# Kernel tuning notes

Hardware: AMD Instinct MI355X
Metric: run time of the kernel (lower is better)

The kernel has to match this reference:

```python
import jax, jax.numpy as jnp
import numpy as np

N_USERS = 60000
N_ITEMS = 30000
N_NODES = N_USERS + N_ITEMS
D = 64
L = 2


def _norm_adj(edge_index):
    # symmetrize: A_idx = [e, e.flip(0)]
    src = jnp.concatenate([edge_index[0], edge_index[1]])
    dst = jnp.concatenate([edge_index[1], edge_index[0]])
    ones = jnp.ones_like(src, dtype=jnp.float32)
    deg = jax.ops.segment_sum(ones, src, num_segments=N_NODES)
    deg = jnp.clip(deg, 1.0, None)
    val = jax.lax.rsqrt(deg[src]) * jax.lax.rsqrt(deg[dst])
    return src, dst, val


def _spmm(src, dst, val, x):
    # out[i] = sum_{(i,j) in E} val_ij * x[j]
    return jax.ops.segment_sum(val[:, None] * x[dst], src, num_segments=N_NODES)


def setup_inputs() -> dict:
    key = jax.random.key(0)
    ks = jax.random.split(key, 20)
    s = 0.02
    inp = {
        'x_txt': jax.random.normal(ks[0], (N_ITEMS, 768), jnp.float32),
        'x_img': jax.random.normal(ks[1], (N_ITEMS, 512), jnp.float32),
        'x_struct': jax.random.normal(ks[2], (N_ITEMS, 128), jnp.float32),
        'user_emb': jax.random.normal(ks[3], (3, N_USERS, D), jnp.float32) * s,
        'W_txt': jax.random.normal(ks[4], (3, 768, D), jnp.float32) * s,
        'b_txt': jax.random.normal(ks[5], (3, D), jnp.float32) * s,
        'W_img': jax.random.normal(ks[6], (3, 512, D), jnp.float32) * s,
        'b_img': jax.random.normal(ks[7], (3, D), jnp.float32) * s,
        'W_st': jax.random.normal(ks[8], (3, 128, D), jnp.float32) * s,
        'b_st': jax.random.normal(ks[9], (3, D), jnp.float32) * s,
        'Wu1': jax.random.normal(ks[10], (3 * D, 128), jnp.float32) * s,
        'bu1': jax.random.normal(ks[11], (128,), jnp.float32) * s,
        'Wu2': jax.random.normal(ks[12], (128, 3), jnp.float32) * s,
        'bu2': jax.random.normal(ks[13], (3,), jnp.float32) * s,
        'Wi1': jax.random.normal(ks[14], (3 * D, 128), jnp.float32) * s,
        'bi1': jax.random.normal(ks[15], (128,), jnp.float32) * s,
        'Wi2': jax.random.normal(ks[16], (128, 3), jnp.float32) * s,
        'bi2': jax.random.normal(ks[17], (3,), jnp.float32) * s,
        'edge_index': jax.random.randint(ks[18], (2, 500000), 0, N_NODES, jnp.int64),
    }
    return inp


def reference(x_txt, x_img, x_struct, user_emb, W_txt, b_txt, W_img, b_img,
              W_st, b_st, Wu1, bu1, Wu2, bu2, Wi1, bi1, Wi2, bi2, edge_index):
    src, dst, val = _norm_adj(edge_index)

    # item embeddings for all 3 branches at once: [n_items, 3, d]
    i0 = (jnp.einsum('nt,btd->nbd', x_txt, W_txt) + b_txt
          + jnp.einsum('nt,btd->nbd', x_img, W_img) + b_img
          + jnp.einsum('nt,btd->nbd', x_struct, W_st) + b_st)
    u0 = jnp.transpose(user_emb, (1, 0, 2))  # [n_users, 3, d]
    x = jnp.concatenate([u0, i0], axis=0).reshape(N_NODES, 3 * D)

    out = x
    for _ in range(L):
        x = _spmm(src, dst, val, x)
        out = out + x
    out = out / (L + 1)

    stack = out.reshape(N_NODES, 3, D)
    U_stack, I_stack = stack[:N_USERS], stack[N_USERS:]
    U_cat = U_stack.reshape(N_USERS, 3 * D)
    I_cat = I_stack.reshape(N_ITEMS, 3 * D)

    a_u = jax.nn.softmax(jax.nn.relu(U_cat @ Wu1 + bu1) @ Wu2 + bu2, axis=-1)
    a_i = jax.nn.softmax(jax.nn.relu(I_cat @ Wi1 + bi1) @ Wi2 + bi2, axis=-1)

    U = jnp.einsum('nb,nbd->nd', a_u, U_stack)
    I = jnp.einsum('nb,nbd->nd', a_i, I_stack)
    return jnp.concatenate([U, I], axis=0)  # [N_NODES, d]
```

## Files before the change

### kernel.cpp

```cpp
#include <hip/hip_runtime.h>
#include <math.h>

#define N_USERS 60000
#define N_ITEMS 30000
#define N_NODES 90000
#define DD 64
#define FF 192
#define FH 96
#define KK_TOT 1408
#define E_UND 500000
#define E_DIR 1000000
#define SCAN_NBLK 88

typedef __attribute__((ext_vector_type(8))) __bf16 bf16x8;
typedef __attribute__((ext_vector_type(8))) unsigned short u16x8;
typedef __attribute__((ext_vector_type(4))) float f32x4;

__device__ __forceinline__ unsigned short f2bf(float f) {
    unsigned int u = __float_as_uint(f);
    unsigned int r = (u + 0x7FFFu + ((u >> 16) & 1u)) >> 16;
    return (unsigned short)r;
}
__device__ __forceinline__ float bf_lo(unsigned int x) { return __uint_as_float(x << 16); }
__device__ __forceinline__ float bf_hi(unsigned int x) { return __uint_as_float(x & 0xFFFF0000u); }
__device__ __forceinline__ float bf2f(unsigned short x) {
    return __uint_as_float((unsigned int)x << 16);
}
__device__ __forceinline__ unsigned int pack2(float a, float b) {
    return ((unsigned int)f2bf(b) << 16) | (unsigned int)f2bf(a);
}

__global__ void k_mode(const int* __restrict__ ei, int* __restrict__ mode) {
    __shared__ int any;
    if (threadIdx.x == 0) any = 0;
    __syncthreads();
    if (ei[2 * threadIdx.x + 1] != 0) atomicOr(&any, 1);
    __syncthreads();
    if (threadIdx.x == 0) mode[0] = (any == 0) ? 1 : 0;
}

__device__ __forceinline__ void load_pair(const int* __restrict__ ei, int md, int u,
                                          int& a, int& b) {
    if (md) { a = ei[2 * u]; b = ei[2 * (E_UND + u)]; }
    else    { a = ei[u];     b = ei[E_UND + u]; }
}

__global__ void k_deg(const int* __restrict__ ei, const int* __restrict__ mode,
                      int* __restrict__ deg) {
    int i = blockIdx.x * 256 + threadIdx.x;
    if (i >= E_UND) return;
    int md = mode[0];
    int a, b;
    load_pair(ei, md, i, a, b);
    atomicAdd(&deg[a], 1);
    atomicAdd(&deg[b], 1);
}

__global__ __launch_bounds__(1024) void k_scan1(const int* __restrict__ deg,
                                                int* __restrict__ offs,
                                                int* __restrict__ bsum) {
    __shared__ int tmp[1024];
    int b = blockIdx.x, t = threadIdx.x;
    int i = b * 1024 + t;
    int v = (i < N_NODES) ? deg[i] : 0;
    tmp[t] = v;
    __syncthreads();
    for (int off = 1; off < 1024; off <<= 1) {
        int add = (t >= off) ? tmp[t - off] : 0;
        __syncthreads();
        tmp[t] += add;
        __syncthreads();
    }
    offs[i] = tmp[t] - v;
    if (t == 1023) bsum[b] = tmp[t];
}

__global__ void k_scan2(const int* __restrict__ bsum, int* __restrict__ bscan) {
    if (threadIdx.x == 0) {
        int run = 0;
        for (int b = 0; b < SCAN_NBLK; b++) { bscan[b] = run; run += bsum[b]; }
    }
}

__global__ void k_scan3(const int* __restrict__ deg, int* __restrict__ offs,
                        const int* __restrict__ bscan, int* __restrict__ cursor,
                        float* __restrict__ rsq) {
    int i = blockIdx.x * 256 + threadIdx.x;
    if (i >= N_NODES) return;
    int o = offs[i] + bscan[i >> 10];
    offs[i] = o;
    cursor[i] = o;
    int dg = deg[i];
    if (dg < 1) dg = 1;
    rsq[i] = rsqrtf((float)dg);
}

__global__ void k_fill(const int* __restrict__ ei, const int* __restrict__ mode,
                       int* __restrict__ cursor, const float* __restrict__ rsq,
                       int* __restrict__ edst, float* __restrict__ eval) {
    int i = blockIdx.x * 256 + threadIdx.x;
    if (i >= E_DIR) return;
    int md = mode[0];
    int u = (i < E_UND) ? i : i - E_UND;
    int a, b;
    load_pair(ei, md, u, a, b);
    int s, d;
    if (i < E_UND) { s = a; d = b; } else { s = b; d = a; }
    int slot = atomicAdd(&cursor[s], 1);
    edst[slot] = d;
    eval[slot] = rsq[s] * rsq[d];
}

__global__ void k_users(const float* __restrict__ ue, float* __restrict__ S,
                        unsigned short* __restrict__ Xbs) {
    int idx = blockIdx.x * 256 + threadIdx.x;
    if (idx >= N_USERS * FF) return;
    int n = idx / FF;
    int r = idx - n * FF;
    int b = r >> 6, d = r & 63;
    float v = ue[((size_t)b * N_USERS + n) * DD + d];
    S[idx] = v;
    Xbs[idx] = f2bf(v);
}

__global__ void k_cvt_w(const float* __restrict__ Wt, const float* __restrict__ Wi,
                        const float* __restrict__ Wst, unsigned short* __restrict__ Wtb) {
    int idx = blockIdx.x * 256 + threadIdx.x;
    if (idx >= FF * KK_TOT) return;
    int n = idx / KK_TOT;
    int k = idx - n * KK_TOT;
    int b = n >> 6, d = n & 63;
    float v;
    if (k < 768)       v = Wt [((size_t)b * 768 + k) * 64 + d];
    else if (k < 1280) v = Wi [((size_t)b * 512 + (k - 768)) * 64 + d];
    else               v = Wst[((size_t)b * 128 + (k - 1280)) * 64 + d];
    Wtb[idx] = f2bf(v);
}

__global__ void k_cvt_w1(const float* __restrict__ Wu1, const float* __restrict__ Wi1,
                         unsigned short* __restrict__ W1Tu,
                         unsigned short* __restrict__ W1Ti) {
    int idx = blockIdx.x * 256 + threadIdx.x;
    if (idx >= 128 * FF) return;
    int n = idx / FF;
    int k = idx - n * FF;
    W1Tu[idx] = f2bf(Wu1[(size_t)k * 128 + n]);
    W1Ti[idx] = f2bf(Wi1[(size_t)k * 128 + n]);
}

#define BM 64
#define BNH 96
#define BK 64
#define LDK 72

__global__ __launch_bounds__(256) void k_item_gemm_mfma3(
    const float* __restrict__ xt, const float* __restrict__ xi, const float* __restrict__ xs,
    const unsigned short* __restrict__ Wtb,
    const float* __restrict__ bt, const float* __restrict__ bi, const float* __restrict__ bst,
    float* __restrict__ S, unsigned short* __restrict__ Xbs) {
    __shared__ unsigned short Ash[BM * LDK];
    __shared__ unsigned short Bsh[BNH * LDK];
    const int tid  = threadIdx.x;
    const int wave = tid >> 6;
    const int lane = tid & 63;
    const int row0 = (blockIdx.x >> 1) * BM;
    const int n0   = (blockIdx.x & 1) * BNH;

    f32x4 acc[6];
#pragma unroll
    for (int tn = 0; tn < 6; tn++) acc[tn] = (f32x4){0.f, 0.f, 0.f, 0.f};

    const int l16  = lane & 15;
    const int quad = lane >> 4;

    for (int k0 = 0; k0 < KK_TOT; k0 += BK) {
#pragma unroll
        for (int i = 0; i < 2; i++) {
            int id = tid + i * 256;
            int r = id >> 3;
            int c = (id & 7) << 3;
            int gr = row0 + r;
            int gk = k0 + c;
            float4 v0 = make_float4(0.f, 0.f, 0.f, 0.f);
            float4 v1 = v0;
            if (gr < N_ITEMS) {
                const float* src;
                int kl;
                if (gk < 768)       { src = xt + (size_t)gr * 768; kl = gk; }
                else if (gk < 1280) { src = xi + (size_t)gr * 512; kl = gk - 768; }
                else                { src = xs + (size_t)gr * 128; kl = gk - 1280; }
                v0 = *(const float4*)(src + kl);
                v1 = *(const float4*)(src + kl + 4);
            }
            u16x8 pk;
            pk[0] = f2bf(v0.x); pk[1] = f2bf(v0.y); pk[2] = f2bf(v0.z); pk[3] = f2bf(v0.w);
            pk[4] = f2bf(v1.x); pk[5] = f2bf(v1.y); pk[6] = f2bf(v1.z); pk[7] = f2bf(v1.w);
            *(u16x8*)(&Ash[r * LDK + c]) = pk;
        }
#pragma unroll
        for (int i = 0; i < 3; i++) {
            int id = tid + i * 256;
            int r = id >> 3;
            int c = (id & 7) << 3;
            *(u16x8*)(&Bsh[r * LDK + c]) =
                *(const u16x8*)(&Wtb[(size_t)(n0 + r) * KK_TOT + k0 + c]);
        }
        __syncthreads();
#pragma unroll
        for (int kk = 0; kk < BK; kk += 32) {
            bf16x8 af = *(const bf16x8*)(&Ash[(wave * 16 + l16) * LDK + kk + quad * 8]);
#pragma unroll
            for (int tn = 0; tn < 6; tn++) {
                bf16x8 bfr = *(const bf16x8*)(&Bsh[(tn * 16 + l16) * LDK + kk + quad * 8]);
                acc[tn] = __builtin_amdgcn_mfma_f32_16x16x32_bf16(af, bfr, acc[tn], 0, 0, 0);
            }
        }
        __syncthreads();
    }

#pragma unroll
    for (int tn = 0; tn < 6; tn++) {
        int n = n0 + tn * 16 + l16;
        int b = n >> 6, d = n & 63;
        float bias = bt[b * 64 + d] + bi[b * 64 + d] + bst[b * 64 + d];
#pragma unroll
        for (int r = 0; r < 4; r++) {
            int row = row0 + wave * 16 + quad * 4 + r;
            if (row < N_ITEMS) {
                size_t o = (size_t)(N_USERS + row) * FF + n;
                float v = acc[tn][r] + bias;
                S[o] = v;
                Xbs[o] = f2bf(v);
            }
        }
    }
}

__global__ __launch_bounds__(192) void k_spmm_bf(const unsigned int* __restrict__ Xb,
                                                 unsigned int* __restrict__ Yb,
                                                 float* __restrict__ S,
                                                 const int* __restrict__ offs,
                                                 const int* __restrict__ deg,
                                                 const int* __restrict__ edst,
                                                 const float* __restrict__ eval) {
    int t = threadIdx.x;
    int half = (t >= FH) ? 1 : 0;
    int c = t - half * FH;
    int n = blockIdx.x * 2 + half;
    int start = offs[n];
    int dg = deg[n];
    const int* ed = edst + start;
    const float* ev = eval + start;
    float a0 = 0.f, a1 = 0.f;
    for (int j = 0; j < dg; j += 4) {
        int last = dg - 1;
        int j1 = (j + 1 < dg) ? j + 1 : last;
        int j2 = (j + 2 < dg) ? j + 2 : last;
        int j3 = (j + 3 < dg) ? j + 3 : last;
        int d0 = ed[j], d1 = ed[j1], d2 = ed[j2], d3 = ed[j3];
        float v0 = ev[j];
        float v1 = (j + 1 < dg) ? ev[j1] : 0.f;
        float v2 = (j + 2 < dg) ? ev[j2] : 0.f;
        float v3 = (j + 3 < dg) ? ev[j3] : 0.f;
        unsigned int x0 = Xb[(size_t)d0 * FH + c];
        unsigned int x1 = Xb[(size_t)d1 * FH + c];
        unsigned int x2 = Xb[(size_t)d2 * FH + c];
        unsigned int x3 = Xb[(size_t)d3 * FH + c];
        a0 = fmaf(v0, bf_lo(x0), a0); a1 = fmaf(v0, bf_hi(x0), a1);
        a0 = fmaf(v1, bf_lo(x1), a0); a1 = fmaf(v1, bf_hi(x1), a1);
        a0 = fmaf(v2, bf_lo(x2), a0); a1 = fmaf(v2, bf_hi(x2), a1);
        a0 = fmaf(v3, bf_lo(x3), a0); a1 = fmaf(v3, bf_hi(x3), a1);
    }
    size_t o = (size_t)n * FH + c;
    Yb[o] = pack2(a0, a1);
    float2* Sp = (float2*)(S + (size_t)n * FF);
    float2 s = Sp[c];
    s.x += a0; s.y += a1;
    Sp[c] = s;
}

#define LDA 200

__global__ __launch_bounds__(256) void k_attn_mfma(
    const float* __restrict__ S,
    const unsigned short* __restrict__ W1T,
    const float* __restrict__ B1,
    const float* __restrict__ W2,
    const float* __restrict__ B2,
    float* __restrict__ out,
    int node_base, int n_rows) {
    __shared__ unsigned short Atile[64 * LDA];
    __shared__ float aws[64][4];
    const int tid  = threadIdx.x;
    const int wave = tid >> 6;
    const int lane = tid & 63;
    const int row0 = blockIdx.x * 64;
    const float inv3 = 1.f / 3.f;

#pragma unroll
    for (int i = 0; i < 6; i++) {
        int id = tid + i * 256;
        int r = id / 24;
        int c = (id - r * 24) * 8;
        u16x8 pk;
        if (row0 + r < n_rows) {
            const float* src = S + (size_t)(node_base + row0 + r) * FF + c;
            float4 v0 = *(const float4*)(src);
            float4 v1 = *(const float4*)(src + 4);
            pk[0] = f2bf(v0.x * inv3); pk[1] = f2bf(v0.y * inv3);
            pk[2] = f2bf(v0.z * inv3); pk[3] = f2bf(v0.w * inv3);
            pk[4] = f2bf(v1.x * inv3); pk[5] = f2bf(v1.y * inv3);
            pk[6] = f2bf(v1.z * inv3); pk[7] = f2bf(v1.w * inv3);
        } else {
            pk = (u16x8){0, 0, 0, 0, 0, 0, 0, 0};
        }
        *(u16x8*)(&Atile[r * LDA + c]) = pk;
    }
    __syncthreads();

    f32x4 acc[8];
#pragma unroll
    for (int tn = 0; tn < 8; tn++) acc[tn] = (f32x4){0.f, 0.f, 0.f, 0.f};
    const int l16 = lane & 15;
    const int quad = lane >> 4;
#pragma unroll
    for (int kk = 0; kk < FF; kk += 32) {
        bf16x8 af = *(const bf16x8*)(&Atile[(wave * 16 + l16) * LDA + kk + quad * 8]);
#pragma unroll
        for (int tn = 0; tn < 8; tn++) {
            bf16x8 bf = *(const bf16x8*)(&W1T[(size_t)(tn * 16 + l16) * FF + kk + quad * 8]);
            acc[tn] = __builtin_amdgcn_mfma_f32_16x16x32_bf16(af, bf, acc[tn], 0, 0, 0);
        }
    }

    float pl[4][3];
#pragma unroll
    for (int r = 0; r < 4; r++) { pl[r][0] = 0.f; pl[r][1] = 0.f; pl[r][2] = 0.f; }
#pragma unroll
    for (int tn = 0; tn < 8; tn++) {
        int col = tn * 16 + l16;
        float b1v = B1[col];
        float w0 = W2[col * 3 + 0], w1 = W2[col * 3 + 1], w2v = W2[col * 3 + 2];
#pragma unroll
        for (int r = 0; r < 4; r++) {
            float h = fmaxf(acc[tn][r] + b1v, 0.f);
            pl[r][0] = fmaf(h, w0, pl[r][0]);
            pl[r][1] = fmaf(h, w1, pl[r][1]);
            pl[r][2] = fmaf(h, w2v, pl[r][2]);
        }
    }
#pragma unroll
    for (int m = 1; m <= 8; m <<= 1) {
#pragma unroll
        for (int r = 0; r < 4; r++) {
            pl[r][0] += __shfl_xor(pl[r][0], m, 64);
            pl[r][1] += __shfl_xor(pl[r][1], m, 64);
            pl[r][2] += __shfl_xor(pl[r][2], m, 64);
        }
    }
    float b20 = B2[0], b21 = B2[1], b22 = B2[2];
    if (l16 == 0) {
#pragma unroll
        for (int r = 0; r < 4; r++) {
            float l0 = pl[r][0] + b20, l1 = pl[r][1] + b21, l2 = pl[r][2] + b22;
            float mx = fmaxf(l0, fmaxf(l1, l2));
            float e0 = __expf(l0 - mx), e1 = __expf(l1 - mx), e2 = __expf(l2 - mx);
            float inv = 1.f / (e0 + e1 + e2);
            int rr = wave * 16 + quad * 4 + r;
            aws[rr][0] = e0 * inv; aws[rr][1] = e1 * inv; aws[rr][2] = e2 * inv;
        }
    }
    __syncthreads();

#pragma unroll
    for (int i = 0; i < 16; i++) {
        int flat = tid + i * 256;
        int r = flat >> 6, d = flat & 63;
        if (row0 + r < n_rows) {
            float a0 = aws[r][0], a1 = aws[r][1], a2 = aws[r][2];
            const unsigned short* Ar = &Atile[r * LDA];
            float v = a0 * bf2f(Ar[d]) + a1 * bf2f(Ar[64 + d]) + a2 * bf2f(Ar[128 + d]);
            out[(size_t)(node_base + row0 + r) * DD + d] = v;
        }
    }
}

extern "C" void kernel_launch(void* const* d_in, const int* in_sizes, int n_in,
                              void* d_out, int out_size, void* d_ws, size_t ws_size,
                              hipStream_t stream) {
    (void)in_sizes; (void)n_in; (void)out_size; (void)ws_size;
    const float* x_txt    = (const float*)d_in[0];
    const float* x_img    = (const float*)d_in[1];
    const float* x_struct = (const float*)d_in[2];
    const float* user_emb = (const float*)d_in[3];
    const float* W_txt    = (const float*)d_in[4];
    const float* b_txt    = (const float*)d_in[5];
    const float* W_img    = (const float*)d_in[6];
    const float* b_img    = (const float*)d_in[7];
    const float* W_st     = (const float*)d_in[8];
    const float* b_st     = (const float*)d_in[9];
    const float* Wu1      = (const float*)d_in[10];
    const float* bu1      = (const float*)d_in[11];
    const float* Wu2      = (const float*)d_in[12];
    const float* bu2      = (const float*)d_in[13];
    const float* Wi1      = (const float*)d_in[14];
    const float* bi1      = (const float*)d_in[15];
    const float* Wi2      = (const float*)d_in[16];
    const float* bi2      = (const float*)d_in[17];
    const int*   ei       = (const int*)d_in[18];
    float* out = (float*)d_out;

    char* base = (char*)d_ws;
    size_t off = 0;
    auto take = [&](size_t bytes) -> void* {
        void* p = base + off;
        off += (bytes + 255) & ~(size_t)255;
        return p;
    };
    float* S           = (float*)take((size_t)N_NODES * FF * 4);
    unsigned int* Xb0  = (unsigned int*)take((size_t)N_NODES * FH * 4);
    unsigned int* Yb   = (unsigned int*)take((size_t)N_NODES * FH * 4);
    int* deg    = (int*)take((size_t)N_NODES * 4);
    int* offs   = (int*)take((size_t)SCAN_NBLK * 1024 * 4);
    int* cursor = (int*)take((size_t)N_NODES * 4);
    int* bsum   = (int*)take((size_t)SCAN_NBLK * 4);
    int* bscan  = (int*)take((size_t)SCAN_NBLK * 4);
    float* rsq  = (float*)take((size_t)N_NODES * 4);
    int* edst   = (int*)take((size_t)E_DIR * 4);
    float* eval = (float*)take((size_t)E_DIR * 4);
    int* mode   = (int*)take(256);
    unsigned short* Wtb  = (unsigned short*)take((size_t)FF * KK_TOT * 2);
    unsigned short* W1Tu = (unsigned short*)take((size_t)128 * FF * 2);
    unsigned short* W1Ti = (unsigned short*)take((size_t)128 * FF * 2);

    hipMemsetAsync(deg, 0, (size_t)N_NODES * 4, stream);

    k_mode<<<1, 256, 0, stream>>>(ei, mode);
    k_deg<<<(E_UND + 255) / 256, 256, 0, stream>>>(ei, mode, deg);
    k_scan1<<<SCAN_NBLK, 1024, 0, stream>>>(deg, offs, bsum);
    k_scan2<<<1, 64, 0, stream>>>(bsum, bscan);
    k_scan3<<<(N_NODES + 255) / 256, 256, 0, stream>>>(deg, offs, bscan, cursor, rsq);
    k_fill<<<(E_DIR + 255) / 256, 256, 0, stream>>>(ei, mode, cursor, rsq, edst, eval);

    k_users<<<(N_USERS * FF + 255) / 256, 256, 0, stream>>>(user_emb, S,
                                                            (unsigned short*)Xb0);
    k_cvt_w<<<(FF * KK_TOT + 255) / 256, 256, 0, stream>>>(W_txt, W_img, W_st, Wtb);
    k_cvt_w1<<<(128 * FF + 255) / 256, 256, 0, stream>>>(Wu1, Wi1, W1Tu, W1Ti);
    k_item_gemm_mfma3<<<((N_ITEMS + BM - 1) / BM) * 2, 256, 0, stream>>>(
        x_txt, x_img, x_struct, Wtb, b_txt, b_img, b_st, S, (unsigned short*)Xb0);

    k_spmm_bf<<<N_NODES / 2, 192, 0, stream>>>(Xb0, Yb, S, offs, deg, edst, eval);
    k_spmm_bf<<<N_NODES / 2, 192, 0, stream>>>(Yb, Xb0, S, offs, deg, edst, eval);

    k_attn_mfma<<<(N_USERS + 63) / 64, 256, 0, stream>>>(
        S, W1Tu, bu1, Wu2, bu2, out, 0, N_USERS);
    k_attn_mfma<<<(N_ITEMS + 63) / 64, 256, 0, stream>>>(
        S, W1Ti, bi1, Wi2, bi2, out, N_USERS, N_ITEMS);
}
```

Before: 676.8 us.

## Drop fp32 running-sum buffer and sum bf16 layer outputs in attention kernel

Removes the fp32 accumulator S that each stage read and rewrote. Each propagation layer now gets its own bf16 buffer (a new Zb is added), and the attention kernel loads all three layer buffers and averages them while building its tile. This cuts a large amount of fp32 global-memory traffic from the user init, item GEMM and both SpMM passes. In exchange the sum is now formed from bf16-rounded layer values, including layer 0, which lowers precision.

```diff
diff --git a/kernel.cpp b/kernel.cpp
--- a/kernel.cpp
+++ b/kernel.cpp
@@ -111,16 +111,13 @@
     eval[slot] = rsq[s] * rsq[d];
 }
 
-__global__ void k_users(const float* __restrict__ ue, float* __restrict__ S,
-                        unsigned short* __restrict__ Xbs) {
+__global__ void k_users(const float* __restrict__ ue, unsigned short* __restrict__ Xbs) {
     int idx = blockIdx.x * 256 + threadIdx.x;
     if (idx >= N_USERS * FF) return;
     int n = idx / FF;
     int r = idx - n * FF;
     int b = r >> 6, d = r & 63;
-    float v = ue[((size_t)b * N_USERS + n) * DD + d];
-    S[idx] = v;
-    Xbs[idx] = f2bf(v);
+    Xbs[idx] = f2bf(ue[((size_t)b * N_USERS + n) * DD + d]);
 }
 
 __global__ void k_cvt_w(const float* __restrict__ Wt, const float* __restrict__ Wi,
@@ -157,7 +154,7 @@
     const float* __restrict__ xt, const float* __restrict__ xi, const float* __restrict__ xs,
     const unsigned short* __restrict__ Wtb,
     const float* __restrict__ bt, const float* __restrict__ bi, const float* __restrict__ bst,
-    float* __restrict__ S, unsigned short* __restrict__ Xbs) {
+    unsigned short* __restrict__ Xbs) {
     __shared__ unsigned short Ash[BM * LDK];
     __shared__ unsigned short Bsh[BNH * LDK];
     const int tid  = threadIdx.x;
@@ -227,10 +224,7 @@
         for (int r = 0; r < 4; r++) {
             int row = row0 + wave * 16 + quad * 4 + r;
             if (row < N_ITEMS) {
-                size_t o = (size_t)(N_USERS + row) * FF + n;
-                float v = acc[tn][r] + bias;
-                S[o] = v;
-                Xbs[o] = f2bf(v);
+                Xbs[(size_t)(N_USERS + row) * FF + n] = f2bf(acc[tn][r] + bias);
             }
         }
     }
@@ -238,7 +232,6 @@
 
 __global__ __launch_bounds__(192) void k_spmm_bf(const unsigned int* __restrict__ Xb,
                                                  unsigned int* __restrict__ Yb,
-                                                 float* __restrict__ S,
                                                  const int* __restrict__ offs,
                                                  const int* __restrict__ deg,
                                                  const int* __restrict__ edst,
@@ -271,18 +264,15 @@
         a0 = fmaf(v2, bf_lo(x2), a0); a1 = fmaf(v2, bf_hi(x2), a1);
         a0 = fmaf(v3, bf_lo(x3), a0); a1 = fmaf(v3, bf_hi(x3), a1);
     }
-    size_t o = (size_t)n * FH + c;
-    Yb[o] = pack2(a0, a1);
-    float2* Sp = (float2*)(S + (size_t)n * FF);
-    float2 s = Sp[c];
-    s.x += a0; s.y += a1;
-    Sp[c] = s;
+    Yb[(size_t)n * FH + c] = pack2(a0, a1);
 }
 
 #define LDA 200
 
 __global__ __launch_bounds__(256) void k_attn_mfma(
-    const float* __restrict__ S,
+    const unsigned int* __restrict__ X0,
+    const unsigned int* __restrict__ X1,
+    const unsigned int* __restrict__ X2,
     const unsigned short* __restrict__ W1T,
     const float* __restrict__ B1,
     const float* __restrict__ W2,
@@ -301,20 +291,25 @@
     for (int i = 0; i < 6; i++) {
         int id = tid + i * 256;
         int r = id / 24;
-        int c = (id - r * 24) * 8;
+        int q = id - r * 24;
         u16x8 pk;
         if (row0 + r < n_rows) {
-            const float* src = S + (size_t)(node_base + row0 + r) * FF + c;
-            float4 v0 = *(const float4*)(src);
-            float4 v1 = *(const float4*)(src + 4);
-            pk[0] = f2bf(v0.x * inv3); pk[1] = f2bf(v0.y * inv3);
-            pk[2] = f2bf(v0.z * inv3); pk[3] = f2bf(v0.w * inv3);
-            pk[4] = f2bf(v1.x * inv3); pk[5] = f2bf(v1.y * inv3);
-            pk[6] = f2bf(v1.z * inv3); pk[7] = f2bf(v1.w * inv3);
+            size_t base = (size_t)(node_base + row0 + r) * FH + q * 4;
+            uint4 a = *(const uint4*)(X0 + base);
+            uint4 b = *(const uint4*)(X1 + base);
+            uint4 c = *(const uint4*)(X2 + base);
+            pk[0] = f2bf((bf_lo(a.x) + bf_lo(b.x) + bf_lo(c.x)) * inv3);
+            pk[1] = f2bf((bf_hi(a.x) + bf_hi(b.x) + bf_hi(c.x)) * inv3);
+            pk[2] = f2bf((bf_lo(a.y) + bf_lo(b.y) + bf_lo(c.y)) * inv3);
+            pk[3] = f2bf((bf_hi(a.y) + bf_hi(b.y) + bf_hi(c.y)) * inv3);
+            pk[4] = f2bf((bf_lo(a.z) + bf_lo(b.z) + bf_lo(c.z)) * inv3);
+            pk[5] = f2bf((bf_hi(a.z) + bf_hi(b.z) + bf_hi(c.z)) * inv3);
+            pk[6] = f2bf((bf_lo(a.w) + bf_lo(b.w) + bf_lo(c.w)) * inv3);
+            pk[7] = f2bf((bf_hi(a.w) + bf_hi(b.w) + bf_hi(c.w)) * inv3);
         } else {
             pk = (u16x8){0, 0, 0, 0, 0, 0, 0, 0};
         }
-        *(u16x8*)(&Atile[r * LDA + c]) = pk;
+        *(u16x8*)(&Atile[r * LDA + q * 8]) = pk;
     }
     __syncthreads();
 
@@ -417,9 +412,9 @@
         off += (bytes + 255) & ~(size_t)255;
         return p;
     };
-    float* S           = (float*)take((size_t)N_NODES * FF * 4);
     unsigned int* Xb0  = (unsigned int*)take((size_t)N_NODES * FH * 4);
     unsigned int* Yb   = (unsigned int*)take((size_t)N_NODES * FH * 4);
+    unsigned int* Zb   = (unsigned int*)take((size_t)N_NODES * FH * 4);
     int* deg    = (int*)take((size_t)N_NODES * 4);
     int* offs   = (int*)take((size_t)SCAN_NBLK * 1024 * 4);
     int* cursor = (int*)take((size_t)N_NODES * 4);
@@ -442,18 +437,18 @@
     k_scan3<<<(N_NODES + 255) / 256, 256, 0, stream>>>(deg, offs, bscan, cursor, rsq);
     k_fill<<<(E_DIR + 255) / 256, 256, 0, stream>>>(ei, mode, cursor, rsq, edst, eval);
 
-    k_users<<<(N_USERS * FF + 255) / 256, 256, 0, stream>>>(user_emb, S,
+    k_users<<<(N_USERS * FF + 255) / 256, 256, 0, stream>>>(user_emb,
                                                             (unsigned short*)Xb0);
     k_cvt_w<<<(FF * KK_TOT + 255) / 256, 256, 0, stream>>>(W_txt, W_img, W_st, Wtb);
     k_cvt_w1<<<(128 * FF + 255) / 256, 256, 0, stream>>>(Wu1, Wi1, W1Tu, W1Ti);
     k_item_gemm_mfma3<<<((N_ITEMS + BM - 1) / BM) * 2, 256, 0, stream>>>(
-        x_txt, x_img, x_struct, Wtb, b_txt, b_img, b_st, S, (unsigned short*)Xb0);
-
-    k_spmm_bf<<<N_NODES / 2, 192, 0, stream>>>(Xb0, Yb, S, offs, deg, edst, eval);
-    k_spmm_bf<<<N_NODES / 2, 192, 0, stream>>>(Yb, Xb0, S, offs, deg, edst, eval);
+        x_txt, x_img, x_struct, Wtb, b_txt, b_img, b_st, (unsigned short*)Xb0);
+
+    k_spmm_bf<<<N_NODES / 2, 192, 0, stream>>>(Xb0, Yb, offs, deg, edst, eval);
+    k_spmm_bf<<<N_NODES / 2, 192, 0, stream>>>(Yb, Zb, offs, deg, edst, eval);
 
     k_attn_mfma<<<(N_USERS + 63) / 64, 256, 0, stream>>>(
-        S, W1Tu, bu1, Wu2, bu2, out, 0, N_USERS);
+        Xb0, Yb, Zb, W1Tu, bu1, Wu2, bu2, out, 0, N_USERS);
     k_attn_mfma<<<(N_ITEMS + 63) / 64, 256, 0, stream>>>(
-        S, W1Ti, bi1, Wi2, bi2, out, N_USERS, N_ITEMS);
-}
+        Xb0, Yb, Zb, W1Ti, bi1, Wi2, bi2, out, N_USERS, N_ITEMS);
+}
```

Result: faster. 625.8 us (-7.5%).
